# Performance work log

Hardware: AMD Instinct MI355X
Metric: run time of the kernel (lower is better)

Reference implementation:

```python
import jax, jax.numpy as jnp
import numpy as np

B, T, J, C = 32, 256, 21, 3
BT = B * T
N = BT * J

_TPL_SRC = np.array([0, 1, 2, 3, 4, 0, 5, 6, 7, 8, 0, 9, 10, 11, 12, 0, 13, 14, 15, 16, 0, 17, 18, 19, 20], np.int32)
_TPL_DST = np.array([1, 2, 3, 4, 0, 5, 6, 7, 8, 0, 9, 10, 11, 12, 0, 13, 14, 15, 16, 0, 17, 18, 19, 20, 0], np.int32)


def _build_edges():
    off = (np.arange(BT, dtype=np.int32) * J)[:, None]
    src = (_TPL_SRC[None, :] + off).ravel()
    dst = (_TPL_DST[None, :] + off).ravel()
    # PyG GATConv default add_self_loops=True (both layers see the same augmented set)
    loops = np.arange(N, dtype=np.int32)
    return np.concatenate([src, loops]), np.concatenate([dst, loops])


def setup_inputs() -> dict:
    key = jax.random.key(0)
    ks = jax.random.split(key, 8)
    src, dst = _build_edges()
    return {
        "keypoints": jax.random.normal(ks[0], (B, T, J, C), jnp.float32),
        "W1": jax.random.normal(ks[1], (3, 256), jnp.float32) * 0.3,
        "att1_src": jax.random.normal(ks[2], (4, 64), jnp.float32) * 0.1,
        "att1_dst": jax.random.normal(ks[3], (4, 64), jnp.float32) * 0.1,
        "b1": jnp.zeros((256,), jnp.float32),
        "W2": jax.random.normal(ks[4], (256, 128), jnp.float32) * 0.06,
        "att2_src": jax.random.normal(ks[5], (1, 128), jnp.float32) * 0.1,
        "att2_dst": jax.random.normal(ks[6], (1, 128), jnp.float32) * 0.1,
        "b2": jnp.zeros((128,), jnp.float32),
        "src": jnp.asarray(src),
        "dst": jnp.asarray(dst),
    }


def _gat_conv(x, src, dst, W, a_src, a_dst, b, heads, d_head):
    n = x.shape[0]
    h = (x @ W).reshape(n, heads, d_head)            # [N,H,D]
    e_s = jnp.einsum('nhd,hd->nh', h, a_src)          # [N,H]
    e_d = jnp.einsum('nhd,hd->nh', h, a_dst)
    e = jax.nn.leaky_relu(e_s[src] + e_d[dst], 0.2)   # [E,H]
    m = jax.ops.segment_max(e, dst, num_segments=n)
    ex = jnp.exp(e - m[dst])
    z = jax.ops.segment_sum(ex, dst, num_segments=n)
    alpha = ex / z[dst]                               # scatter-softmax over dst
    out = jax.ops.segment_sum(h[src] * alpha[:, :, None], dst, num_segments=n)
    return out.reshape(n, heads * d_head) + b


def reference(keypoints, W1, att1_src, att1_dst, b1, W2, att2_src, att2_dst, b2, src, dst):
    x = keypoints.reshape(N, C)
    x = jax.nn.relu(_gat_conv(x, src, dst, W1, att1_src, att1_dst, b1, 4, 64))
    x = jax.nn.relu(_gat_conv(x, src, dst, W2, att2_src, att2_dst, b2, 1, 128))
    x = x.reshape(BT, J, 128).mean(axis=1)            # pool joints
    return x.reshape(B, T, 128).mean(axis=1)          # pool time -> [B,128]
```

## Files before the change

kernel.cpp:

```cpp
#include <hip/hip_runtime.h>

#define NJ  21
#define X1S 264
#define H2S 136

typedef __attribute__((ext_vector_type(8))) short  bf16x8;
typedef __attribute__((ext_vector_type(4))) float  floatx4;

__device__ __forceinline__ float lrelu(float v){ return v > 0.f ? v : 0.2f*v; }
__device__ __forceinline__ unsigned short f2bf(float x){
  unsigned int u = __float_as_uint(x);
  return (unsigned short)((u + 0x7FFFu + ((u >> 16) & 1u)) >> 16);
}
__device__ __forceinline__ float bf2f(unsigned short h){
  return __uint_as_float(((unsigned int)h) << 16);
}

__global__ void prep(const float* __restrict__ W1, const float* __restrict__ a1s,
                     const float* __restrict__ a1d, const float* __restrict__ W2,
                     unsigned short* __restrict__ w2f, float* __restrict__ ws1o){
  int t = threadIdx.x;
  int base = blockIdx.x*1024 + t*4;
  #pragma unroll
  for (int i = 0; i < 4; ++i){
    int idx = base + i;
    int j = idx & 7, lane = (idx >> 3) & 63, nt = (idx >> 9) & 7, kt = idx >> 12;
    int k = kt*32 + (lane >> 4)*8 + j;
    int n = nt*16 + (lane & 15);
    w2f[idx] = f2bf(W2[k*128 + n]);
  }
  if (blockIdx.x == 0 && t < 24){
    int c = t % 3, h = (t/3) & 3, sd = t/12;
    const float* av = sd ? a1d : a1s;
    float s = 0.f;
    #pragma unroll
    for (int d = 0; d < 64; ++d) s += W1[c*256 + h*64 + d]*av[h*64 + d];
    ws1o[sd*12 + c*4 + h] = s;
  }
}

__global__ __launch_bounds__(256, 6)
void gat_fused(const float* __restrict__ kp,  const float* __restrict__ W1,
               const float* __restrict__ b1v, const float* __restrict__ a2s,
               const float* __restrict__ a2d, const float* __restrict__ b2v,
               const unsigned short* __restrict__ w2f, const float* __restrict__ ws1g,
               float* __restrict__ out)
{
  __shared__ float xs[NJ][3];
  __shared__ float es1[NJ][4], ed1[NJ][4];
  __shared__ float xag[NJ][4][4];
  __shared__ unsigned short x1bf[32*X1S];
  __shared__ unsigned short h2bf[NJ*H2S];
  __shared__ float ps2[NJ][4], pd2[NJ][4];
  __shared__ float es2[NJ], ed2[NJ];
  __shared__ float al2[NJ][6];

  const int t = threadIdx.x;

  if (t < NJ*3) xs[t/3][t%3] = kp[(long)blockIdx.x*(NJ*3) + t];
  __syncthreads();

  if (t < NJ*4){
    int n = t >> 2, h = t & 3;
    float s = 0.f, d = 0.f;
    #pragma unroll
    for (int c = 0; c < 3; ++c){
      float xv = xs[n][c];
      s += xv * ws1g[c*4 + h];
      d += xv * ws1g[12 + c*4 + h];
    }
    es1[n][h] = s; ed1[n][h] = d;
  }
  __syncthreads();

  if (t < NJ*4){
    int n = t >> 2, h = t & 3;
    int p[6], np;
    if (n == 0){ p[0]=4;p[1]=8;p[2]=12;p[3]=16;p[4]=20;p[5]=0; np=6; }
    else       { p[0]=(n%4==1)?0:(n-1); p[1]=n; np=2; }
    float ed = ed1[n][h];
    float e[6], m = -1e30f;
    for (int i = 0; i < np; ++i){ e[i] = lrelu(es1[p[i]][h] + ed); m = fmaxf(m, e[i]); }
    float z = 0.f;
    for (int i = 0; i < np; ++i){ e[i] = __expf(e[i] - m); z += e[i]; }
    float inv = 1.f/z;
    float a0=0.f, a1=0.f, a2=0.f;
    for (int i = 0; i < np; ++i){
      float al = e[i]*inv; int s = p[i];
      a0 += al*xs[s][0]; a1 += al*xs[s][1]; a2 += al*xs[s][2];
    }
    xag[n][h][0]=a0; xag[n][h][1]=a1; xag[n][h][2]=a2;
  }
  __syncthreads();

  for (int o = t; o < 32*64; o += 256){
    int n = o >> 6, kq = o & 63, k = kq*4;
    unsigned short us0=0, us1=0, us2=0, us3=0;
    if (n < NJ){
      int h = kq >> 4;
      float xa0 = xag[n][h][0], xa1 = xag[n][h][1], xa2 = xag[n][h][2];
      float4 bb = *(const float4*)(b1v + k);
      float4 w0 = *(const float4*)(W1 + k);
      float4 w1 = *(const float4*)(W1 + 256 + k);
      float4 w2 = *(const float4*)(W1 + 512 + k);
      us0 = f2bf(fmaxf(bb.x + xa0*w0.x + xa1*w1.x + xa2*w2.x, 0.f));
      us1 = f2bf(fmaxf(bb.y + xa0*w0.y + xa1*w1.y + xa2*w2.y, 0.f));
      us2 = f2bf(fmaxf(bb.z + xa0*w0.z + xa1*w1.z + xa2*w2.z, 0.f));
      us3 = f2bf(fmaxf(bb.w + xa0*w0.w + xa1*w1.w + xa2*w2.w, 0.f));
    }
    uint2 pk;
    pk.x = (unsigned)us0 | ((unsigned)us1 << 16);
    pk.y = (unsigned)us2 | ((unsigned)us3 << 16);
    *(uint2*)&x1bf[n*X1S + k] = pk;
  }
  __syncthreads();

  {
    const int w = t >> 6, lane = t & 63;
    const int ln15 = lane & 15, quad = lane >> 4;
    floatx4 acc00 = {0.f,0.f,0.f,0.f}, acc01 = acc00, acc10 = acc00, acc11 = acc00;
    const unsigned ao0 = (unsigned)(ln15*X1S + quad*8);
    const unsigned ao1 = (unsigned)((16 + ln15)*X1S + quad*8);
    #pragma unroll
    for (int kt = 0; kt < 8; ++kt){
      bf16x8 a0 = *(bf16x8*)&x1bf[ao0 + kt*32];
      bf16x8 a1 = *(bf16x8*)&x1bf[ao1 + kt*32];
      bf16x8 b0 = *(const bf16x8*)(w2f + (unsigned)((kt*8 + 2*w    )*64 + lane)*8);
      bf16x8 b1 = *(const bf16x8*)(w2f + (unsigned)((kt*8 + 2*w + 1)*64 + lane)*8);
      acc00 = __builtin_amdgcn_mfma_f32_16x16x32_bf16(a0, b0, acc00, 0, 0, 0);
      acc01 = __builtin_amdgcn_mfma_f32_16x16x32_bf16(a0, b1, acc01, 0, 0, 0);
      acc10 = __builtin_amdgcn_mfma_f32_16x16x32_bf16(a1, b0, acc10, 0, 0, 0);
      acc11 = __builtin_amdgcn_mfma_f32_16x16x32_bf16(a1, b1, acc11, 0, 0, 0);
    }
    const int c0 = w*32 + ln15, c1 = w*32 + 16 + ln15;
    #pragma unroll
    for (int r = 0; r < 4; ++r){
      int row0 = quad*4 + r;
      h2bf[row0*H2S + c0] = f2bf(acc00[r]);
      h2bf[row0*H2S + c1] = f2bf(acc01[r]);
      int row1 = 16 + quad*4 + r;
      if (row1 < NJ){
        h2bf[row1*H2S + c0] = f2bf(acc10[r]);
        h2bf[row1*H2S + c1] = f2bf(acc11[r]);
      }
    }
  }
  __syncthreads();

  if (t < NJ*4){
    int n = t >> 2, q = t & 3;
    float s = 0.f, d = 0.f;
    #pragma unroll
    for (int j = 0; j < 32; ++j){
      float hv = bf2f(h2bf[n*H2S + q*32 + j]);
      s += hv * a2s[q*32 + j];
      d += hv * a2d[q*32 + j];
    }
    ps2[n][q] = s; pd2[n][q] = d;
  }
  __syncthreads();
  if (t < NJ){
    es2[t] = ps2[t][0] + ps2[t][1] + ps2[t][2] + ps2[t][3];
    ed2[t] = pd2[t][0] + pd2[t][1] + pd2[t][2] + pd2[t][3];
  }
  __syncthreads();
  if (t < NJ){
    int n = t;
    int p[6], np;
    if (n == 0){ p[0]=4;p[1]=8;p[2]=12;p[3]=16;p[4]=20;p[5]=0; np=6; }
    else       { p[0]=(n%4==1)?0:(n-1); p[1]=n; np=2; }
    float ed = ed2[n];
    float e[6], m = -1e30f;
    for (int i = 0; i < np; ++i){ e[i] = lrelu(es2[p[i]] + ed); m = fmaxf(m, e[i]); }
    float z = 0.f;
    for (int i = 0; i < np; ++i){ e[i] = __expf(e[i] - m); z += e[i]; }
    float inv = 1.f/z;
    for (int i = 0; i < np; ++i) al2[n][i] = e[i]*inv;
  }
  __syncthreads();

  if (t < 128){
    int j = t;
    float bj = b2v[j];
    float sum = 0.f;
    {
      float v = bj + al2[0][0]*bf2f(h2bf[ 4*H2S + j]) + al2[0][1]*bf2f(h2bf[ 8*H2S + j])
                   + al2[0][2]*bf2f(h2bf[12*H2S + j]) + al2[0][3]*bf2f(h2bf[16*H2S + j])
                   + al2[0][4]*bf2f(h2bf[20*H2S + j]) + al2[0][5]*bf2f(h2bf[ 0*H2S + j]);
      sum += fmaxf(v, 0.f);
    }
    #pragma unroll
    for (int n = 1; n < NJ; ++n){
      int p = (n%4==1) ? 0 : (n-1);
      float v = bj + al2[n][0]*bf2f(h2bf[p*H2S + j]) + al2[n][1]*bf2f(h2bf[n*H2S + j]);
      sum += fmaxf(v, 0.f);
    }
    atomicAdd(&out[(blockIdx.x >> 8)*128 + j], sum*(1.f/5376.f));
  }
}

extern "C" void kernel_launch(void* const* d_in, const int* in_sizes, int n_in,
                              void* d_out, int out_size, void* d_ws, size_t ws_size,
                              hipStream_t stream){
  const float* kp  = (const float*)d_in[0];
  const float* W1  = (const float*)d_in[1];
  const float* a1s = (const float*)d_in[2];
  const float* a1d = (const float*)d_in[3];
  const float* b1  = (const float*)d_in[4];
  const float* W2  = (const float*)d_in[5];
  const float* a2s = (const float*)d_in[6];
  const float* a2d = (const float*)d_in[7];
  const float* b2  = (const float*)d_in[8];
  float* out = (float*)d_out;

  unsigned short* w2f = (unsigned short*)d_ws;
  float* ws1 = (float*)((char*)d_ws + 65536);

  hipMemsetAsync(out, 0, (size_t)out_size*sizeof(float), stream);
  prep<<<32, 256, 0, stream>>>(W1, a1s, a1d, W2, w2f, ws1);
  gat_fused<<<8192, 256, 0, stream>>>(kp, W1, b1, a2s, a2d, b2, w2f, ws1, out);
}
```

Baseline: 158.1 us.

## Process eight frames per block with register-resident W2 fragments and fused prep

Each block now handles 8 frames (two per iteration across four iterations) instead of one. The W2 bf16 B-fragments are loaded and converted once per block into registers, and the per-head attention projections are computed in-block, so the separate prep kernel goes away. This amortizes weight loads, launch overhead and atomics across more work, and fills a third MFMA row tile by packing two frames (42 rows) into the 48-row LDS tile. In exchange, each block reads W2 from global memory with strided scalar loads and carries heavy register pressure at reduced occupancy (launch_bounds 256,3), with only 1024 blocks.

Result: slower. 179.6 us (+13.6%).

```diff
diff --git a/kernel.cpp b/kernel.cpp
--- a/kernel.cpp
+++ b/kernel.cpp
@@ -16,187 +16,213 @@
   return __uint_as_float(((unsigned int)h) << 16);
 }
 
-__global__ void prep(const float* __restrict__ W1, const float* __restrict__ a1s,
-                     const float* __restrict__ a1d, const float* __restrict__ W2,
-                     unsigned short* __restrict__ w2f, float* __restrict__ ws1o){
-  int t = threadIdx.x;
-  int base = blockIdx.x*1024 + t*4;
-  #pragma unroll
-  for (int i = 0; i < 4; ++i){
-    int idx = base + i;
-    int j = idx & 7, lane = (idx >> 3) & 63, nt = (idx >> 9) & 7, kt = idx >> 12;
-    int k = kt*32 + (lane >> 4)*8 + j;
-    int n = nt*16 + (lane & 15);
-    w2f[idx] = f2bf(W2[k*128 + n]);
-  }
-  if (blockIdx.x == 0 && t < 24){
-    int c = t % 3, h = (t/3) & 3, sd = t/12;
+__global__ __launch_bounds__(256, 3)
+void gat_fused(const float* __restrict__ kp,  const float* __restrict__ W1,
+               const float* __restrict__ a1s, const float* __restrict__ a1d,
+               const float* __restrict__ b1v, const float* __restrict__ W2,
+               const float* __restrict__ a2s, const float* __restrict__ a2d,
+               const float* __restrict__ b2v, float* __restrict__ out)
+{
+  __shared__ float xsL[8][NJ][4];
+  __shared__ float wsl[2][12];
+  __shared__ float xagL[4][42][4];
+  __shared__ unsigned short x1bf[48*X1S];
+  __shared__ unsigned short h2bf[42*H2S];
+  __shared__ float a2sL[128], a2dL[128];
+  __shared__ float es2[42], ed2[42];
+  __shared__ float al2L[42][8];
+  __shared__ float pool2[256];
+
+  const int t    = threadIdx.x;
+  const int blk  = blockIdx.x;
+  const int w    = t >> 6, lane = t & 63, quad = lane >> 4, ln15 = lane & 15;
+
+  for (int o = t; o < 504; o += 256){
+    int f = o/63, r = o%63;
+    xsL[f][r/3][r%3] = kp[blk*504 + o];
+  }
+  if (t < 128){ a2sL[t] = a2s[t]; a2dL[t] = a2d[t]; }
+  if (t < 24){
+    int c = t%3, h = (t/3)&3, sd = t/12;
     const float* av = sd ? a1d : a1s;
     float s = 0.f;
     #pragma unroll
     for (int d = 0; d < 64; ++d) s += W1[c*256 + h*64 + d]*av[h*64 + d];
-    ws1o[sd*12 + c*4 + h] = s;
-  }
-}
-
-__global__ __launch_bounds__(256, 6)
-void gat_fused(const float* __restrict__ kp,  const float* __restrict__ W1,
-               const float* __restrict__ b1v, const float* __restrict__ a2s,
-               const float* __restrict__ a2d, const float* __restrict__ b2v,
-               const unsigned short* __restrict__ w2f, const float* __restrict__ ws1g,
-               float* __restrict__ out)
-{
-  __shared__ float xs[NJ][3];
-  __shared__ float es1[NJ][4], ed1[NJ][4];
-  __shared__ float xag[NJ][4][4];
-  __shared__ unsigned short x1bf[32*X1S];
-  __shared__ unsigned short h2bf[NJ*H2S];
-  __shared__ float ps2[NJ][4], pd2[NJ][4];
-  __shared__ float es2[NJ], ed2[NJ];
-  __shared__ float al2[NJ][6];
-
-  const int t = threadIdx.x;
-
-  if (t < NJ*3) xs[t/3][t%3] = kp[(long)blockIdx.x*(NJ*3) + t];
-  __syncthreads();
-
-  if (t < NJ*4){
-    int n = t >> 2, h = t & 3;
-    float s = 0.f, d = 0.f;
-    #pragma unroll
-    for (int c = 0; c < 3; ++c){
-      float xv = xs[n][c];
-      s += xv * ws1g[c*4 + h];
-      d += xv * ws1g[12 + c*4 + h];
-    }
-    es1[n][h] = s; ed1[n][h] = d;
-  }
-  __syncthreads();
-
-  if (t < NJ*4){
-    int n = t >> 2, h = t & 3;
-    int p[6], np;
-    if (n == 0){ p[0]=4;p[1]=8;p[2]=12;p[3]=16;p[4]=20;p[5]=0; np=6; }
-    else       { p[0]=(n%4==1)?0:(n-1); p[1]=n; np=2; }
-    float ed = ed1[n][h];
-    float e[6], m = -1e30f;
-    for (int i = 0; i < np; ++i){ e[i] = lrelu(es1[p[i]][h] + ed); m = fmaxf(m, e[i]); }
-    float z = 0.f;
-    for (int i = 0; i < np; ++i){ e[i] = __expf(e[i] - m); z += e[i]; }
-    float inv = 1.f/z;
-    float a0=0.f, a1=0.f, a2=0.f;
-    for (int i = 0; i < np; ++i){
-      float al = e[i]*inv; int s = p[i];
-      a0 += al*xs[s][0]; a1 += al*xs[s][1]; a2 += al*xs[s][2];
-    }
-    xag[n][h][0]=a0; xag[n][h][1]=a1; xag[n][h][2]=a2;
-  }
-  __syncthreads();
-
-  for (int o = t; o < 32*64; o += 256){
-    int n = o >> 6, kq = o & 63, k = kq*4;
-    unsigned short us0=0, us1=0, us2=0, us3=0;
-    if (n < NJ){
-      int h = kq >> 4;
-      float xa0 = xag[n][h][0], xa1 = xag[n][h][1], xa2 = xag[n][h][2];
-      float4 bb = *(const float4*)(b1v + k);
-      float4 w0 = *(const float4*)(W1 + k);
-      float4 w1 = *(const float4*)(W1 + 256 + k);
-      float4 w2 = *(const float4*)(W1 + 512 + k);
-      us0 = f2bf(fmaxf(bb.x + xa0*w0.x + xa1*w1.x + xa2*w2.x, 0.f));
-      us1 = f2bf(fmaxf(bb.y + xa0*w0.y + xa1*w1.y + xa2*w2.y, 0.f));
-      us2 = f2bf(fmaxf(bb.z + xa0*w0.z + xa1*w1.z + xa2*w2.z, 0.f));
-      us3 = f2bf(fmaxf(bb.w + xa0*w0.w + xa1*w1.w + xa2*w2.w, 0.f));
-    }
-    uint2 pk;
-    pk.x = (unsigned)us0 | ((unsigned)us1 << 16);
-    pk.y = (unsigned)us2 | ((unsigned)us3 << 16);
-    *(uint2*)&x1bf[n*X1S + k] = pk;
-  }
-  __syncthreads();
-
+    wsl[sd][c*4+h] = s;
+  }
+
+  bf16x8 Bf0[8], Bf1[8];
   {
-    const int w = t >> 6, lane = t & 63;
-    const int ln15 = lane & 15, quad = lane >> 4;
-    floatx4 acc00 = {0.f,0.f,0.f,0.f}, acc01 = acc00, acc10 = acc00, acc11 = acc00;
-    const unsigned ao0 = (unsigned)(ln15*X1S + quad*8);
-    const unsigned ao1 = (unsigned)((16 + ln15)*X1S + quad*8);
+    const int n0 = 2*w*16 + ln15, n1 = n0 + 16;
     #pragma unroll
     for (int kt = 0; kt < 8; ++kt){
-      bf16x8 a0 = *(bf16x8*)&x1bf[ao0 + kt*32];
-      bf16x8 a1 = *(bf16x8*)&x1bf[ao1 + kt*32];
-      bf16x8 b0 = *(const bf16x8*)(w2f + (unsigned)((kt*8 + 2*w    )*64 + lane)*8);
-      bf16x8 b1 = *(const bf16x8*)(w2f + (unsigned)((kt*8 + 2*w + 1)*64 + lane)*8);
-      acc00 = __builtin_amdgcn_mfma_f32_16x16x32_bf16(a0, b0, acc00, 0, 0, 0);
-      acc01 = __builtin_amdgcn_mfma_f32_16x16x32_bf16(a0, b1, acc01, 0, 0, 0);
-      acc10 = __builtin_amdgcn_mfma_f32_16x16x32_bf16(a1, b0, acc10, 0, 0, 0);
-      acc11 = __builtin_amdgcn_mfma_f32_16x16x32_bf16(a1, b1, acc11, 0, 0, 0);
-    }
-    const int c0 = w*32 + ln15, c1 = w*32 + 16 + ln15;
+      bf16x8 b0, b1;
+      #pragma unroll
+      for (int j = 0; j < 8; ++j){
+        int krow = kt*32 + quad*8 + j;
+        b0[j] = (short)f2bf(W2[krow*128 + n0]);
+        b1[j] = (short)f2bf(W2[krow*128 + n1]);
+      }
+      Bf0[kt] = b0; Bf1[kt] = b1;
+    }
+  }
+
+  const int kc = (t & 127)*2;
+  const float2 w1c0 = *(const float2*)(W1 + kc);
+  const float2 w1c1 = *(const float2*)(W1 + 256 + kc);
+  const float2 w1c2 = *(const float2*)(W1 + 512 + kc);
+  const float2 bbc  = *(const float2*)(b1v + kc);
+  const float  bj   = b2v[t & 127];
+
+  __syncthreads();
+
+  float wsr[3], wdr[3];
+  { int h = t & 3;
     #pragma unroll
-    for (int r = 0; r < 4; ++r){
-      int row0 = quad*4 + r;
-      h2bf[row0*H2S + c0] = f2bf(acc00[r]);
-      h2bf[row0*H2S + c1] = f2bf(acc01[r]);
-      int row1 = 16 + quad*4 + r;
-      if (row1 < NJ){
-        h2bf[row1*H2S + c0] = f2bf(acc10[r]);
-        h2bf[row1*H2S + c1] = f2bf(acc11[r]);
-      }
-    }
-  }
+    for (int c = 0; c < 3; ++c){ wsr[c] = wsl[0][c*4+h]; wdr[c] = wsl[1][c*4+h]; } }
+
+  float poolacc = 0.f;
+
+  for (int it = 0; it < 4; ++it){
+    __syncthreads();
+
+    if (t < 168){
+      int fn = t >> 2;
+      int fl = fn >= NJ ? 1 : 0;
+      int n  = fn - fl*NJ;
+      int f8 = it*2 + fl;
+      int p[6], np;
+      if (n == 0){ p[0]=4;p[1]=8;p[2]=12;p[3]=16;p[4]=20;p[5]=0; np=6; }
+      else       { p[0]=(n%4==1)?0:(n-1); p[1]=n; np=2; }
+      float4 xself = *(const float4*)&xsL[f8][n][0];
+      float ed = xself.x*wdr[0] + xself.y*wdr[1] + xself.z*wdr[2];
+      float4 xp[6]; float e[6]; float m = -1e30f;
+      for (int i = 0; i < np; ++i){
+        xp[i] = *(const float4*)&xsL[f8][p[i]][0];
+        float es = xp[i].x*wsr[0] + xp[i].y*wsr[1] + xp[i].z*wsr[2];
+        e[i] = lrelu(es + ed); m = fmaxf(m, e[i]);
+      }
+      float z = 0.f;
+      for (int i = 0; i < np; ++i){ e[i] = __expf(e[i]-m); z += e[i]; }
+      float inv = 1.f/z;
+      float a0 = 0.f, a1 = 0.f, a2v = 0.f;
+      for (int i = 0; i < np; ++i){
+        float al = e[i]*inv;
+        a0 += al*xp[i].x; a1 += al*xp[i].y; a2v += al*xp[i].z;
+      }
+      *(float4*)&xagL[t & 3][fn][0] = make_float4(a0, a1, a2v, 0.f);
+    }
+    __syncthreads();
+
+    if (t < 128){
+      int h = kc >> 6;
+      for (int r = 0; r < 42; ++r){
+        float4 xa = *(const float4*)&xagL[h][r][0];
+        float v0 = bbc.x + xa.x*w1c0.x + xa.y*w1c1.x + xa.z*w1c2.x;
+        float v1 = bbc.y + xa.x*w1c0.y + xa.y*w1c1.y + xa.z*w1c2.y;
+        unsigned pk = (unsigned)f2bf(fmaxf(v0,0.f)) | ((unsigned)f2bf(fmaxf(v1,0.f)) << 16);
+        *(unsigned*)&x1bf[r*X1S + kc] = pk;
+      }
+    }
+    __syncthreads();
+
+    {
+      floatx4 acc[3][2];
+      #pragma unroll
+      for (int mt = 0; mt < 3; ++mt){ acc[mt][0] = (floatx4){0.f,0.f,0.f,0.f}; acc[mt][1] = acc[mt][0]; }
+      #pragma unroll
+      for (int kt = 0; kt < 8; ++kt){
+        bf16x8 a0 = *(bf16x8*)&x1bf[(     ln15)*X1S + kt*32 + quad*8];
+        bf16x8 a1 = *(bf16x8*)&x1bf[(16 + ln15)*X1S + kt*32 + quad*8];
+        bf16x8 a2 = *(bf16x8*)&x1bf[(32 + ln15)*X1S + kt*32 + quad*8];
+        acc[0][0] = __builtin_amdgcn_mfma_f32_16x16x32_bf16(a0, Bf0[kt], acc[0][0], 0,0,0);
+        acc[0][1] = __builtin_amdgcn_mfma_f32_16x16x32_bf16(a0, Bf1[kt], acc[0][1], 0,0,0);
+        acc[1][0] = __builtin_amdgcn_mfma_f32_16x16x32_bf16(a1, Bf0[kt], acc[1][0], 0,0,0);
+        acc[1][1] = __builtin_amdgcn_mfma_f32_16x16x32_bf16(a1, Bf1[kt], acc[1][1], 0,0,0);
+        acc[2][0] = __builtin_amdgcn_mfma_f32_16x16x32_bf16(a2, Bf0[kt], acc[2][0], 0,0,0);
+        acc[2][1] = __builtin_amdgcn_mfma_f32_16x16x32_bf16(a2, Bf1[kt], acc[2][1], 0,0,0);
+      }
+      const int c0 = 32*w + ln15, c1 = c0 + 16;
+      #pragma unroll
+      for (int mt = 0; mt < 3; ++mt){
+        #pragma unroll
+        for (int r = 0; r < 4; ++r){
+          int row = mt*16 + quad*4 + r;
+          if (row < 42){
+            h2bf[row*H2S + c0] = f2bf(acc[mt][0][r]);
+            h2bf[row*H2S + c1] = f2bf(acc[mt][1][r]);
+          }
+        }
+      }
+    }
+    __syncthreads();
+
+    if (t < 168){
+      int fn = t >> 2, q = t & 3;
+      float s = 0.f, d = 0.f;
+      #pragma unroll
+      for (int jb = 0; jb < 4; ++jb){
+        bf16x8 hv = *(bf16x8*)&h2bf[fn*H2S + q*32 + jb*8];
+        float4 as0 = *(const float4*)&a2sL[q*32 + jb*8];
+        float4 as1 = *(const float4*)&a2sL[q*32 + jb*8 + 4];
+        float4 ad0 = *(const float4*)&a2dL[q*32 + jb*8];
+        float4 ad1 = *(const float4*)&a2dL[q*32 + jb*8 + 4];
+        float h0 = bf2f((unsigned short)hv[0]), h1 = bf2f((unsigned short)hv[1]);
+        float h2v= bf2f((unsigned short)hv[2]), h3 = bf2f((unsigned short)hv[3]);
+        float h4 = bf2f((unsigned short)hv[4]), h5 = bf2f((unsigned short)hv[5]);
+        float h6 = bf2f((unsigned short)hv[6]), h7 = bf2f((unsigned short)hv[7]);
+        s += h0*as0.x + h1*as0.y + h2v*as0.z + h3*as0.w
+           + h4*as1.x + h5*as1.y + h6*as1.z  + h7*as1.w;
+        d += h0*ad0.x + h1*ad0.y + h2v*ad0.z + h3*ad0.w
+           + h4*ad1.x + h5*ad1.y + h6*ad1.z  + h7*ad1.w;
+      }
+      s += __shfl_xor(s, 1); s += __shfl_xor(s, 2);
+      d += __shfl_xor(d, 1); d += __shfl_xor(d, 2);
+      if (q == 0){ es2[fn] = s; ed2[fn] = d; }
+    }
+    __syncthreads();
+
+    if (t < 42){
+      int fl = t >= NJ ? 1 : 0;
+      int n  = t - fl*NJ, base = fl*NJ;
+      int p[6], np;
+      if (n == 0){ p[0]=4;p[1]=8;p[2]=12;p[3]=16;p[4]=20;p[5]=0; np=6; }
+      else       { p[0]=(n%4==1)?0:(n-1); p[1]=n; np=2; }
+      float ed = ed2[t];
+      float e[6], m = -1e30f;
+      for (int i = 0; i < np; ++i){ e[i] = lrelu(es2[base + p[i]] + ed); m = fmaxf(m, e[i]); }
+      float z = 0.f;
+      for (int i = 0; i < np; ++i){ e[i] = __expf(e[i]-m); z += e[i]; }
+      float inv = 1.f/z;
+      for (int i = 0; i < np; ++i) al2L[t][i] = e[i]*inv;
+    }
+    __syncthreads();
+
+    {
+      int fl = t >> 7, j = t & 127, base = fl*NJ;
+      float h0 = bf2f(h2bf[base*H2S + j]);
+      float v0 = al2L[base][5]*h0;
+      float s = 0.f, hprev = h0;
+      #pragma unroll
+      for (int n = 1; n < NJ; ++n){
+        float hn = bf2f(h2bf[(base+n)*H2S + j]);
+        float pv = ((n & 3) == 1) ? h0 : hprev;
+        float2 al = *(const float2*)&al2L[base+n][0];
+        float v = bj + al.x*pv + al.y*hn;
+        s += fmaxf(v, 0.f);
+        if ((n & 3) == 0) v0 += al2L[base][(n >> 2) - 1]*hn;
+        hprev = hn;
+      }
+      s += fmaxf(bj + v0, 0.f);
+      poolacc += s;
+    }
+  }
+
   __syncthreads();
-
-  if (t < NJ*4){
-    int n = t >> 2, q = t & 3;
-    float s = 0.f, d = 0.f;
-    #pragma unroll
-    for (int j = 0; j < 32; ++j){
-      float hv = bf2f(h2bf[n*H2S + q*32 + j]);
-      s += hv * a2s[q*32 + j];
-      d += hv * a2d[q*32 + j];
-    }
-    ps2[n][q] = s; pd2[n][q] = d;
-  }
+  pool2[t] = poolacc;
   __syncthreads();
-  if (t < NJ){
-    es2[t] = ps2[t][0] + ps2[t][1] + ps2[t][2] + ps2[t][3];
-    ed2[t] = pd2[t][0] + pd2[t][1] + pd2[t][2] + pd2[t][3];
-  }
-  __syncthreads();
-  if (t < NJ){
-    int n = t;
-    int p[6], np;
-    if (n == 0){ p[0]=4;p[1]=8;p[2]=12;p[3]=16;p[4]=20;p[5]=0; np=6; }
-    else       { p[0]=(n%4==1)?0:(n-1); p[1]=n; np=2; }
-    float ed = ed2[n];
-    float e[6], m = -1e30f;
-    for (int i = 0; i < np; ++i){ e[i] = lrelu(es2[p[i]] + ed); m = fmaxf(m, e[i]); }
-    float z = 0.f;
-    for (int i = 0; i < np; ++i){ e[i] = __expf(e[i] - m); z += e[i]; }
-    float inv = 1.f/z;
-    for (int i = 0; i < np; ++i) al2[n][i] = e[i]*inv;
-  }
-  __syncthreads();
-
-  if (t < 128){
-    int j = t;
-    float bj = b2v[j];
-    float sum = 0.f;
-    {
-      float v = bj + al2[0][0]*bf2f(h2bf[ 4*H2S + j]) + al2[0][1]*bf2f(h2bf[ 8*H2S + j])
-                   + al2[0][2]*bf2f(h2bf[12*H2S + j]) + al2[0][3]*bf2f(h2bf[16*H2S + j])
-                   + al2[0][4]*bf2f(h2bf[20*H2S + j]) + al2[0][5]*bf2f(h2bf[ 0*H2S + j]);
-      sum += fmaxf(v, 0.f);
-    }
-    #pragma unroll
-    for (int n = 1; n < NJ; ++n){
-      int p = (n%4==1) ? 0 : (n-1);
-      float v = bj + al2[n][0]*bf2f(h2bf[p*H2S + j]) + al2[n][1]*bf2f(h2bf[n*H2S + j]);
-      sum += fmaxf(v, 0.f);
-    }
-    atomicAdd(&out[(blockIdx.x >> 8)*128 + j], sum*(1.f/5376.f));
-  }
+  if (t < 128)
+    atomicAdd(&out[(blk >> 5)*128 + t], (pool2[t] + pool2[t+128])*(1.f/5376.f));
 }
 
 extern "C" void kernel_launch(void* const* d_in, const int* in_sizes, int n_in,
@@ -212,11 +238,6 @@
   const float* a2d = (const float*)d_in[7];
   const float* b2  = (const float*)d_in[8];
   float* out = (float*)d_out;
-
-  unsigned short* w2f = (unsigned short*)d_ws;
-  float* ws1 = (float*)((char*)d_ws + 65536);
-
   hipMemsetAsync(out, 0, (size_t)out_size*sizeof(float), stream);
-  prep<<<32, 256, 0, stream>>>(W1, a1s, a1d, W2, w2f, ws1);
-  gat_fused<<<8192, 256, 0, stream>>>(kp, W1, b1, a2s, a2d, b2, w2f, ws1, out);
-}
+  gat_fused<<<1024, 256, 0, stream>>>(kp, W1, a1s, a1d, b1, W2, a2s, a2d, b2, out);
+}
```
